# Kernel optimization log

Measured on AMD Instinct MI355X. Metric: run time of the kernel, lower is better.

Reference implementation:

```python
import jax, jax.numpy as jnp
import numpy as np

B, S, D, H, HD = 2, 2048, 1024, 16, 64


def setup_inputs() -> dict:
    key = jax.random.key(0)
    ks = jax.random.split(key, 11)
    scale_in = 1.0 / np.sqrt(D)
    return {
        "query": jax.random.normal(ks[0], (B, S, D), jnp.float32),
        "key": jax.random.normal(ks[1], (B, S, D), jnp.float32),
        "value": jax.random.normal(ks[2], (B, S, D), jnp.float32),
        "Wq": jax.random.normal(ks[3], (H, D, HD), jnp.float32) * scale_in,
        "bq": jax.random.normal(ks[4], (H, HD), jnp.float32) * 0.02,
        "Wk": jax.random.normal(ks[5], (H, D, HD), jnp.float32) * scale_in,
        "bk": jax.random.normal(ks[6], (H, HD), jnp.float32) * 0.02,
        "Wv": jax.random.normal(ks[7], (H, D, HD), jnp.float32) * scale_in,
        "bv": jax.random.normal(ks[8], (H, HD), jnp.float32) * 0.02,
        "Wo": jax.random.normal(ks[9], (D, D), jnp.float32) * scale_in,
        "bo": jax.random.normal(ks[10], (D,), jnp.float32) * 0.02,
    }


def reference(query, key, value, Wq, bq, Wk, bk, Wv, bv, Wo, bo):
    # Per-head projections, batched over heads (equivalent to the ModuleList loop).
    q = jnp.einsum('bsd,hdk->bhsk', query, Wq) + bq[None, :, None, :]   # [B,H,S,HD]
    k = jnp.einsum('bsd,hdk->bhsk', key, Wk) + bk[None, :, None, :]
    v = jnp.einsum('bsd,hdk->bhsk', value, Wv) + bv[None, :, None, :]
    scale = 1.0 / jnp.sqrt(jnp.asarray(q.shape[-1], q.dtype))
    scores = jnp.einsum('bhsk,bhtk->bhst', q, k) * scale                # [B,H,S,S]
    attn = jax.nn.softmax(scores, axis=-1)
    ctx = jnp.einsum('bhst,bhtk->bhsk', attn, v)                        # [B,H,S,HD]
    # Concat heads along last dim: [B,S,H*HD] == [B,S,D]
    x = jnp.transpose(ctx, (0, 2, 1, 3)).reshape(ctx.shape[0], ctx.shape[2], -1)
    return x @ Wo + bo
```

## Files before the change

### kernel.cpp

```cpp
#include <hip/hip_runtime.h>
#include <hip/hip_bf16.h>

typedef __bf16 bf16;
typedef __bf16 bf16x8 __attribute__((ext_vector_type(8)));
typedef __bf16 bf16x4 __attribute__((ext_vector_type(4)));
typedef __bf16 bf16x2 __attribute__((ext_vector_type(2)));
typedef float floatx4 __attribute__((ext_vector_type(4)));
typedef float floatx16 __attribute__((ext_vector_type(16)));

#define B_SZ 2
#define S_LEN 2048
#define D_DIM 1024
#define H_CNT 16
#define HD_DIM 64
#define M_ROWS 4096
#define QSCALE 0.18033688011112042f

__device__ __forceinline__ void async_ld16(const bf16* g, bf16* s) {
    __builtin_amdgcn_global_load_lds((const __attribute__((address_space(1))) void*)g,
                                     (__attribute__((address_space(3))) void*)s, 16, 0, 0);
}

__device__ __forceinline__ floatx4 mfma16(bf16x8 a, bf16x8 b, floatx4 c) {
    return __builtin_amdgcn_mfma_f32_16x16x32_bf16(a, b, c, 0, 0, 0);
}
__device__ __forceinline__ floatx16 mfma32(bf16x8 a, bf16x8 b, floatx16 c) {
    return __builtin_amdgcn_mfma_f32_32x32x16_bf16(a, b, c, 0, 0, 0);
}

struct PrepArgs {
    const float* cast_src[3]; bf16* cast_dst[3];
    const float* w_src[3];    bf16* w_dst[3];
    const float* wo;          bf16* wo_t;
};
__global__ __launch_bounds__(256) void prep(PrepArgs a) {
    __shared__ bf16 tile[32][33];
    const int bx = blockIdx.x, tid = threadIdx.x;
    if (bx < 12288) {
        const int t = bx >> 12, blk = bx & 4095;
        const float* s = a.cast_src[t];
        bf16* d = a.cast_dst[t];
        size_t i = ((size_t)blk * 256 + tid) * 4;
        float4 v = *(const float4*)(s + i);
        bf16x4 o = { (bf16)v.x, (bf16)v.y, (bf16)v.z, (bf16)v.w };
        *(bf16x4*)(d + i) = o;
        return;
    }
    int tx = tid & 31, ty = tid >> 5;
    const float* src; bf16* dst; int r0, c0, C, R;
    if (bx < 15360) {
        int idx = bx - 12288;
        int z = idx >> 6, xy = idx & 63;
        int mat = z >> 4, head = z & 15;
        src = a.w_src[mat] + (size_t)head * D_DIM * HD_DIM;
        dst = a.w_dst[mat] + (size_t)head * D_DIM * HD_DIM;
        r0 = (xy & 31) * 32; c0 = (xy >> 5) * 32; C = HD_DIM; R = D_DIM;
    } else {
        int idx = bx - 15360;
        src = a.wo; dst = a.wo_t;
        r0 = (idx & 31) * 32; c0 = (idx >> 5) * 32; C = D_DIM; R = D_DIM;
    }
#pragma unroll
    for (int i = 0; i < 32; i += 8)
        tile[ty + i][tx] = (bf16)src[(size_t)(r0 + ty + i) * C + c0 + tx];
    __syncthreads();
#pragma unroll
    for (int i = 0; i < 32; i += 8)
        dst[(size_t)(c0 + ty + i) * R + r0 + tx] = tile[tx][ty + i];
}

struct GemmPtrs { const bf16* A; const bf16* BT; const float* bias; bf16* C; float* Cf;
                  float scale; int mode; };
struct GemmArgs { GemmPtrs p[3]; };

__global__ __launch_bounds__(256) void gemm_bt(GemmArgs args) {
    __shared__ __align__(16) bf16 As[128 * 32];
    __shared__ __align__(16) bf16 Bs[128 * 32];
    const GemmPtrs P = args.p[blockIdx.z];
    const int tid = threadIdx.x, wave = tid >> 6, lane = tid & 63;
    const int quad = lane >> 4, l15 = lane & 15;
    const int bm = blockIdx.x * 128, bn = blockIdx.y * 128;
    const int wm = (wave >> 1) * 64, wn = (wave & 1) * 64;

    floatx4 acc[4][4];
#pragma unroll
    for (int i = 0; i < 4; i++)
#pragma unroll
        for (int j = 0; j < 4; j++) acc[i][j] = (floatx4){0.f, 0.f, 0.f, 0.f};

    const int srow = (lane >> 2);
    const int scol = (((lane & 3) ^ ((srow >> 1) & 3)) << 3);
    const int ck = ((quad ^ ((l15 >> 1) & 3)) << 3);
    for (int k0 = 0; k0 < 1024; k0 += 32) {
#pragma unroll
        for (int it = 0; it < 2; ++it) {
            int issue = it * 4 + wave;
            int row = issue * 16 + srow;
            async_ld16(P.A + (size_t)(bm + row) * 1024 + k0 + scol, &As[issue * 512]);
            async_ld16(P.BT + (size_t)(bn + row) * 1024 + k0 + scol, &Bs[issue * 512]);
        }
        __syncthreads();
        bf16x8 af[4], bfr[4];
#pragma unroll
        for (int mi = 0; mi < 4; mi++)
            af[mi] = *(const bf16x8*)&As[(wm + mi * 16 + l15) * 32 + ck];
#pragma unroll
        for (int ni = 0; ni < 4; ni++)
            bfr[ni] = *(const bf16x8*)&Bs[(wn + ni * 16 + l15) * 32 + ck];
#pragma unroll
        for (int mi = 0; mi < 4; mi++)
#pragma unroll
            for (int ni = 0; ni < 4; ni++) acc[mi][ni] = mfma16(af[mi], bfr[ni], acc[mi][ni]);
        __syncthreads();
    }
#pragma unroll
    for (int ni = 0; ni < 4; ni++) {
        int col = bn + wn + ni * 16 + l15;
        float bb = P.bias[col];
#pragma unroll
        for (int mi = 0; mi < 4; mi++) {
#pragma unroll
            for (int r = 0; r < 4; r++) {
                int row = bm + wm + mi * 16 + quad * 4 + r;
                float v = (acc[mi][ni][r] + bb) * P.scale;
                if (P.mode == 0) {
                    P.Cf[(size_t)row * 1024 + col] = v;
                } else {
                    int b = row >> 11, s2 = row & 2047, h = col >> 6, hd = col & 63;
                    if (P.mode == 1)
                        P.C[(((size_t)(b * H_CNT + h)) * S_LEN + s2) * HD_DIM + hd] = (bf16)v;
                    else
                        P.C[(((size_t)(b * H_CNT + h)) * HD_DIM + hd) * S_LEN + s2] = (bf16)v;
                }
            }
        }
    }
}

__global__ __launch_bounds__(256) void attn(const bf16* __restrict__ Qg, const bf16* __restrict__ Kg,
                                            const bf16* __restrict__ Vtg, bf16* __restrict__ ctx) {
    __shared__ __align__(16) bf16 Ks[2][8192];
    __shared__ __align__(16) bf16 Vs[2][8192];
    __shared__ __align__(16) bf16 Ps[4][2048];
    const int tid = threadIdx.x, wave = tid >> 6, lane = tid & 63;
    const int l31 = lane & 31, half = lane >> 5;
    const int bid = blockIdx.x;
    const int bh = (bid >> 1) & 31;
    const int qb = ((bid >> 6) << 1) | (bid & 1);
    const int q0blk = qb * 128;
    const bf16* Kp = Kg + (size_t)bh * S_LEN * HD_DIM;
    const bf16* Vp = Vtg + (size_t)bh * HD_DIM * S_LEN;

#pragma unroll
    for (int it = 0; it < 4; ++it) {
        int i = it * 4 + wave;
        int f = i * 512 + lane * 8;
        int sub = f >> 12, rem = f & 4095;
        int c = rem >> 9, r = (rem >> 3) & 63;
        async_ld16(Kp + (size_t)(sub * 64 + r) * HD_DIM + c * 8, &Ks[0][i * 512]);
        async_ld16(Vp + (size_t)r * S_LEN + sub * 64 + c * 8, &Vs[0][i * 512]);
    }
    bf16x8 qf[4];
    {
        const bf16* qrow = Qg + ((size_t)bh * S_LEN + q0blk + wave * 32 + l31) * HD_DIM;
#pragma unroll
        for (int kb = 0; kb < 4; ++kb)
            qf[kb] = *(const bf16x8*)(qrow + (2 * kb + half) * 8);
    }
    __syncthreads();

    bf16* Pw = Ps[wave];
    float l_i = 0.f;
    floatx16 o0 = {0}, o1 = {0};

    for (int rd = 0; rd < 16; ++rd) {
        const int cur = rd & 1;
        if (rd < 15) {
            int t0n = (rd + 1) * 128;
#pragma unroll
            for (int it = 0; it < 4; ++it) {
                int i = it * 4 + wave;
                int f = i * 512 + lane * 8;
                int sub = f >> 12, rem = f & 4095;
                int c = rem >> 9, r = (rem >> 3) & 63;
                async_ld16(Kp + (size_t)(t0n + sub * 64 + r) * HD_DIM + c * 8, &Ks[cur ^ 1][i * 512]);
                async_ld16(Vp + (size_t)r * S_LEN + t0n + sub * 64 + c * 8, &Vs[cur ^ 1][i * 512]);
            }
        }
#pragma unroll
        for (int sub = 0; sub < 2; ++sub) {
            const bf16* Kt = &Ks[cur][sub * 4096];
            const bf16* Vt = &Vs[cur][sub * 4096];
            floatx16 sc0 = {0}, sc1 = {0};
#pragma unroll
            for (int kb = 0; kb < 4; ++kb) {
                bf16x8 k0 = *(const bf16x8*)&Kt[(2 * kb + half) * 512 + l31 * 8];
                bf16x8 k1 = *(const bf16x8*)&Kt[(2 * kb + half) * 512 + (32 + l31) * 8];
                sc0 = mfma32(k0, qf[kb], sc0);
                sc1 = mfma32(k1, qf[kb], sc1);
            }
            float rs = 0.f;
#pragma unroll
            for (int e = 0; e < 16; e += 2) {
                float p0 = __builtin_amdgcn_exp2f(sc0[e]);
                float p1 = __builtin_amdgcn_exp2f(sc0[e + 1]);
                rs += p0 + p1;
                *(bf16x2*)&Pw[(e >> 2) * 256 + l31 * 8 + (e & 3) + 4 * half] = (bf16x2){(bf16)p0, (bf16)p1};
            }
#pragma unroll
            for (int e = 0; e < 16; e += 2) {
                float p0 = __builtin_amdgcn_exp2f(sc1[e]);
                float p1 = __builtin_amdgcn_exp2f(sc1[e + 1]);
                rs += p0 + p1;
                *(bf16x2*)&Pw[(4 + (e >> 2)) * 256 + l31 * 8 + (e & 3) + 4 * half] = (bf16x2){(bf16)p0, (bf16)p1};
            }
            l_i += rs;
#pragma unroll
            for (int kb = 0; kb < 4; ++kb) {
                bf16x8 pf = *(const bf16x8*)&Pw[(2 * kb + half) * 256 + l31 * 8];
                bf16x8 v0 = *(const bf16x8*)&Vt[(2 * kb + half) * 512 + l31 * 8];
                bf16x8 v1 = *(const bf16x8*)&Vt[(2 * kb + half) * 512 + (32 + l31) * 8];
                o0 = mfma32(v0, pf, o0);
                o1 = mfma32(v1, pf, o1);
            }
        }
        __syncthreads();
    }
    l_i += __shfl_xor(l_i, 32);
    int b = bh >> 4, hh = bh & 15;
    float inv = 1.f / l_i;
#pragma unroll
    for (int s2 = 0; s2 < 2; ++s2) {
        const floatx16 oo = s2 ? o1 : o0;
#pragma unroll
        for (int e = 0; e < 16; ++e) {
            int hd = (e & 3) + 8 * (e >> 2) + 4 * half;
            Pw[l31 * 40 + hd] = (bf16)(oo[e] * inv);
        }
#pragma unroll
        for (int p = 0; p < 2; ++p) {
            int q = p * 16 + (lane >> 2), part = lane & 3;
            bf16x8 v = *(const bf16x8*)&Pw[q * 40 + part * 8];
            int s = q0blk + wave * 32 + q;
            *(bf16x8*)&ctx[((size_t)(b * S_LEN + s)) * D_DIM + hh * 64 + s2 * 32 + part * 8] = v;
        }
    }
}

extern "C" void kernel_launch(void* const* d_in, const int* in_sizes, int n_in,
                              void* d_out, int out_size, void* d_ws, size_t ws_size,
                              hipStream_t stream) {
    const float* query = (const float*)d_in[0];
    const float* key   = (const float*)d_in[1];
    const float* value = (const float*)d_in[2];
    const float* Wq = (const float*)d_in[3];
    const float* bq = (const float*)d_in[4];
    const float* Wk = (const float*)d_in[5];
    const float* bk = (const float*)d_in[6];
    const float* Wv = (const float*)d_in[7];
    const float* bv = (const float*)d_in[8];
    const float* Wo = (const float*)d_in[9];
    const float* bo = (const float*)d_in[10];
    float* out = (float*)d_out;

    bf16* ws = (bf16*)d_ws;
    const size_t ASZ = (size_t)M_ROWS * D_DIM;
    const size_t WSZ = (size_t)H_CNT * D_DIM * HD_DIM;
    const size_t TSZ = (size_t)B_SZ * H_CNT * S_LEN * HD_DIM;
    bf16* Qc  = ws;
    bf16* Kc  = Qc + ASZ;
    bf16* Vc  = Kc + ASZ;
    bf16* WqT = Vc + ASZ;
    bf16* WkT = WqT + WSZ;
    bf16* WvT = WkT + WSZ;
    bf16* WoT = WvT + WSZ;
    bf16* Qb  = WoT + (size_t)D_DIM * D_DIM;
    bf16* Kb  = Qb + TSZ;
    bf16* Vtb = Kb + TSZ;
    bf16* ctx = Vtb + TSZ;

    dim3 blk(256);

    PrepArgs pa;
    pa.cast_src[0] = query; pa.cast_src[1] = key; pa.cast_src[2] = value;
    pa.cast_dst[0] = Qc;    pa.cast_dst[1] = Kc;  pa.cast_dst[2] = Vc;
    pa.w_src[0] = Wq; pa.w_src[1] = Wk; pa.w_src[2] = Wv;
    pa.w_dst[0] = WqT; pa.w_dst[1] = WkT; pa.w_dst[2] = WvT;
    pa.wo = Wo; pa.wo_t = WoT;
    prep<<<dim3(16384), blk, 0, stream>>>(pa);

    GemmArgs qkv;
    qkv.p[0] = {Qc, WqT, bq, Qb, nullptr, QSCALE, 1};
    qkv.p[1] = {Kc, WkT, bk, Kb, nullptr, 1.0f, 1};
    qkv.p[2] = {Vc, WvT, bv, Vtb, nullptr, 1.0f, 2};
    gemm_bt<<<dim3(32, 8, 3), blk, 0, stream>>>(qkv);

    attn<<<dim3(512), blk, 0, stream>>>(Qb, Kb, Vtb, ctx);

    GemmArgs og;
    og.p[0] = {ctx, WoT, bo, nullptr, out, 1.0f, 0};
    og.p[1] = og.p[0]; og.p[2] = og.p[0];
    gemm_bt<<<dim3(32, 8, 1), blk, 0, stream>>>(og);
}
```

Measured before the change: 236.5 us.

## Split attention KV range across two wave groups and keep P in registers

The attention kernel now runs 512 threads per block, and two groups of four waves each process half of the key/value sequence for the same 128 queries, 64 keys per round. Partial outputs and row sums are merged through shared memory at the end. The P matrix is no longer round-tripped through LDS; it is reshaped into MFMA operand layout in registers with v_permlane32_swap. s_setprio hints wrap the MFMA sections. These aim to cut LDS traffic and raise wave-level parallelism, at the cost of a shared-memory reduction epilogue and a sync every smaller step.

```diff
diff --git a/kernel.cpp b/kernel.cpp
--- a/kernel.cpp
+++ b/kernel.cpp
@@ -7,6 +7,7 @@
 typedef __bf16 bf16x2 __attribute__((ext_vector_type(2)));
 typedef float floatx4 __attribute__((ext_vector_type(4)));
 typedef float floatx16 __attribute__((ext_vector_type(16)));
+typedef int intx4 __attribute__((ext_vector_type(4)));
 
 #define B_SZ 2
 #define S_LEN 2048
@@ -26,6 +27,13 @@
 }
 __device__ __forceinline__ floatx16 mfma32(bf16x8 a, bf16x8 b, floatx16 c) {
     return __builtin_amdgcn_mfma_f32_32x32x16_bf16(a, b, c, 0, 0, 0);
+}
+
+__device__ __forceinline__ bf16x8 mkfrag(int a0, int a1, int b0, int b1) {
+    asm("v_permlane32_swap_b32 %0, %1" : "+v"(a0), "+v"(b0));
+    asm("v_permlane32_swap_b32 %0, %1" : "+v"(a1), "+v"(b1));
+    intx4 q = {a0, a1, b0, b1};
+    return __builtin_bit_cast(bf16x8, q);
 }
 
 struct PrepArgs {
@@ -137,112 +145,140 @@
     }
 }
 
-__global__ __launch_bounds__(256) void attn(const bf16* __restrict__ Qg, const bf16* __restrict__ Kg,
-                                            const bf16* __restrict__ Vtg, bf16* __restrict__ ctx) {
-    __shared__ __align__(16) bf16 Ks[2][8192];
-    __shared__ __align__(16) bf16 Vs[2][8192];
-    __shared__ __align__(16) bf16 Ps[4][2048];
+__global__ __launch_bounds__(512, 4) void attn(const bf16* __restrict__ Qg, const bf16* __restrict__ Kg,
+                                               const bf16* __restrict__ Vtg, bf16* __restrict__ ctx) {
+    __shared__ __align__(16) bf16 smem[32768];
     const int tid = threadIdx.x, wave = tid >> 6, lane = tid & 63;
     const int l31 = lane & 31, half = lane >> 5;
+    const int grp = wave >> 2, wg = wave & 3;
     const int bid = blockIdx.x;
     const int bh = (bid >> 1) & 31;
     const int qb = ((bid >> 6) << 1) | (bid & 1);
     const int q0blk = qb * 128;
     const bf16* Kp = Kg + (size_t)bh * S_LEN * HD_DIM;
     const bf16* Vp = Vtg + (size_t)bh * HD_DIM * S_LEN;
-
-#pragma unroll
-    for (int it = 0; it < 4; ++it) {
-        int i = it * 4 + wave;
-        int f = i * 512 + lane * 8;
-        int sub = f >> 12, rem = f & 4095;
-        int c = rem >> 9, r = (rem >> 3) & 63;
-        async_ld16(Kp + (size_t)(sub * 64 + r) * HD_DIM + c * 8, &Ks[0][i * 512]);
-        async_ld16(Vp + (size_t)r * S_LEN + sub * 64 + c * 8, &Vs[0][i * 512]);
-    }
+    const int tbase = grp * 1024;
+
+    const int f0 = wg * 512 + lane * 8, f1 = (wg + 4) * 512 + lane * 8;
+    const int kc0 = f0 >> 9, kt0 = (f0 >> 3) & 63;
+    const int kc1 = f1 >> 9, kt1 = (f1 >> 3) & 63;
+    bf16* const Kbase = smem + grp * 8192;
+    bf16* const Vbase = smem + 16384 + grp * 8192;
+
+#define STAGE(BUF, T0) do { \
+        bf16* Kd = Kbase + (BUF) * 4096; \
+        bf16* Vd = Vbase + (BUF) * 4096; \
+        async_ld16(Kp + (size_t)((T0) + kt0) * HD_DIM + kc0 * 8, Kd + wg * 512); \
+        async_ld16(Kp + (size_t)((T0) + kt1) * HD_DIM + kc1 * 8, Kd + (wg + 4) * 512); \
+        async_ld16(Vp + (size_t)kt0 * S_LEN + (T0) + kc0 * 8, Vd + wg * 512); \
+        async_ld16(Vp + (size_t)kt1 * S_LEN + (T0) + kc1 * 8, Vd + (wg + 4) * 512); \
+    } while (0)
+
+    STAGE(0, tbase);
     bf16x8 qf[4];
     {
-        const bf16* qrow = Qg + ((size_t)bh * S_LEN + q0blk + wave * 32 + l31) * HD_DIM;
+        const bf16* qrow = Qg + ((size_t)bh * S_LEN + q0blk + wg * 32 + l31) * HD_DIM;
 #pragma unroll
         for (int kb = 0; kb < 4; ++kb)
             qf[kb] = *(const bf16x8*)(qrow + (2 * kb + half) * 8);
     }
     __syncthreads();
 
-    bf16* Pw = Ps[wave];
     float l_i = 0.f;
     floatx16 o0 = {0}, o1 = {0};
 
     for (int rd = 0; rd < 16; ++rd) {
         const int cur = rd & 1;
-        if (rd < 15) {
-            int t0n = (rd + 1) * 128;
-#pragma unroll
-            for (int it = 0; it < 4; ++it) {
-                int i = it * 4 + wave;
-                int f = i * 512 + lane * 8;
-                int sub = f >> 12, rem = f & 4095;
-                int c = rem >> 9, r = (rem >> 3) & 63;
-                async_ld16(Kp + (size_t)(t0n + sub * 64 + r) * HD_DIM + c * 8, &Ks[cur ^ 1][i * 512]);
-                async_ld16(Vp + (size_t)r * S_LEN + t0n + sub * 64 + c * 8, &Vs[cur ^ 1][i * 512]);
+        if (rd < 15) STAGE(cur ^ 1, tbase + (rd + 1) * 64);
+        const bf16* Kt = Kbase + cur * 4096;
+        const bf16* Vt = Vbase + cur * 4096;
+        floatx16 sc0 = {0}, sc1 = {0};
+        __builtin_amdgcn_s_setprio(1);
+#pragma unroll
+        for (int kb = 0; kb < 4; ++kb) {
+            bf16x8 k0 = *(const bf16x8*)&Kt[(2 * kb + half) * 512 + l31 * 8];
+            bf16x8 k1 = *(const bf16x8*)&Kt[(2 * kb + half) * 512 + (32 + l31) * 8];
+            sc0 = mfma32(k0, qf[kb], sc0);
+            sc1 = mfma32(k1, qf[kb], sc1);
+        }
+        __builtin_amdgcn_s_setprio(0);
+        float rs = 0.f;
+        int w0[8], w1[8];
+#pragma unroll
+        for (int e = 0; e < 16; e += 2) {
+            float p0 = __builtin_amdgcn_exp2f(sc0[e]);
+            float p1 = __builtin_amdgcn_exp2f(sc0[e + 1]);
+            rs += p0 + p1;
+            bf16x2 t2 = {(bf16)p0, (bf16)p1};
+            w0[e >> 1] = __builtin_bit_cast(int, t2);
+        }
+#pragma unroll
+        for (int e = 0; e < 16; e += 2) {
+            float p0 = __builtin_amdgcn_exp2f(sc1[e]);
+            float p1 = __builtin_amdgcn_exp2f(sc1[e + 1]);
+            rs += p0 + p1;
+            bf16x2 t2 = {(bf16)p0, (bf16)p1};
+            w1[e >> 1] = __builtin_bit_cast(int, t2);
+        }
+        l_i += rs;
+        bf16x8 pfr[4];
+        pfr[0] = mkfrag(w0[0], w0[1], w0[2], w0[3]);
+        pfr[1] = mkfrag(w0[4], w0[5], w0[6], w0[7]);
+        pfr[2] = mkfrag(w1[0], w1[1], w1[2], w1[3]);
+        pfr[3] = mkfrag(w1[4], w1[5], w1[6], w1[7]);
+        __builtin_amdgcn_s_setprio(1);
+#pragma unroll
+        for (int kb = 0; kb < 4; ++kb) {
+            bf16x8 v0 = *(const bf16x8*)&Vt[(2 * kb + half) * 512 + l31 * 8];
+            bf16x8 v1 = *(const bf16x8*)&Vt[(2 * kb + half) * 512 + (32 + l31) * 8];
+            o0 = mfma32(v0, pfr[kb], o0);
+            o1 = mfma32(v1, pfr[kb], o1);
+        }
+        __builtin_amdgcn_s_setprio(0);
+        __syncthreads();
+    }
+#undef STAGE
+
+    l_i += __shfl_xor(l_i, 32);
+
+    float* slabF = (float*)smem;
+    float* lA = slabF + 4 * 2112;
+    if (grp == 0) {
+        float* S0 = slabF + wg * 2112;
+#pragma unroll
+        for (int s2 = 0; s2 < 2; ++s2) {
+            const floatx16 oo = s2 ? o1 : o0;
+#pragma unroll
+            for (int e = 0; e < 16; ++e) {
+                int hd = s2 * 32 + (e & 3) + 8 * (e >> 2) + 4 * half;
+                S0[l31 * 66 + hd] = oo[e];
             }
         }
-#pragma unroll
-        for (int sub = 0; sub < 2; ++sub) {
-            const bf16* Kt = &Ks[cur][sub * 4096];
-            const bf16* Vt = &Vs[cur][sub * 4096];
-            floatx16 sc0 = {0}, sc1 = {0};
-#pragma unroll
-            for (int kb = 0; kb < 4; ++kb) {
-                bf16x8 k0 = *(const bf16x8*)&Kt[(2 * kb + half) * 512 + l31 * 8];
-                bf16x8 k1 = *(const bf16x8*)&Kt[(2 * kb + half) * 512 + (32 + l31) * 8];
-                sc0 = mfma32(k0, qf[kb], sc0);
-                sc1 = mfma32(k1, qf[kb], sc1);
+        if (lane < 32) lA[wg * 32 + l31] = l_i;
+    }
+    __syncthreads();
+    if (grp == 1) {
+        float* S0 = slabF + wg * 2112;
+        float lt = l_i + lA[wg * 32 + l31];
+        float inv = 1.f / lt;
+        int b = bh >> 4, hh = bh & 15;
+        bf16* Sw = smem + 17408 + wg * 1280;
+#pragma unroll
+        for (int s2 = 0; s2 < 2; ++s2) {
+            const floatx16 oo = s2 ? o1 : o0;
+#pragma unroll
+            for (int e = 0; e < 16; ++e) {
+                int hd = (e & 3) + 8 * (e >> 2) + 4 * half;
+                float v = (oo[e] + S0[l31 * 66 + s2 * 32 + hd]) * inv;
+                Sw[l31 * 40 + hd] = (bf16)v;
             }
-            float rs = 0.f;
-#pragma unroll
-            for (int e = 0; e < 16; e += 2) {
-                float p0 = __builtin_amdgcn_exp2f(sc0[e]);
-                float p1 = __builtin_amdgcn_exp2f(sc0[e + 1]);
-                rs += p0 + p1;
-                *(bf16x2*)&Pw[(e >> 2) * 256 + l31 * 8 + (e & 3) + 4 * half] = (bf16x2){(bf16)p0, (bf16)p1};
+#pragma unroll
+            for (int p = 0; p < 2; ++p) {
+                int q = p * 16 + (lane >> 2), part = lane & 3;
+                bf16x8 v = *(const bf16x8*)&Sw[q * 40 + part * 8];
+                int s = q0blk + wg * 32 + q;
+                *(bf16x8*)&ctx[((size_t)(b * S_LEN + s)) * D_DIM + hh * 64 + s2 * 32 + part * 8] = v;
             }
-#pragma unroll
-            for (int e = 0; e < 16; e += 2) {
-                float p0 = __builtin_amdgcn_exp2f(sc1[e]);
-                float p1 = __builtin_amdgcn_exp2f(sc1[e + 1]);
-                rs += p0 + p1;
-                *(bf16x2*)&Pw[(4 + (e >> 2)) * 256 + l31 * 8 + (e & 3) + 4 * half] = (bf16x2){(bf16)p0, (bf16)p1};
-            }
-            l_i += rs;
-#pragma unroll
-            for (int kb = 0; kb < 4; ++kb) {
-                bf16x8 pf = *(const bf16x8*)&Pw[(2 * kb + half) * 256 + l31 * 8];
-                bf16x8 v0 = *(const bf16x8*)&Vt[(2 * kb + half) * 512 + l31 * 8];
-                bf16x8 v1 = *(const bf16x8*)&Vt[(2 * kb + half) * 512 + (32 + l31) * 8];
-                o0 = mfma32(v0, pf, o0);
-                o1 = mfma32(v1, pf, o1);
-            }
-        }
-        __syncthreads();
-    }
-    l_i += __shfl_xor(l_i, 32);
-    int b = bh >> 4, hh = bh & 15;
-    float inv = 1.f / l_i;
-#pragma unroll
-    for (int s2 = 0; s2 < 2; ++s2) {
-        const floatx16 oo = s2 ? o1 : o0;
-#pragma unroll
-        for (int e = 0; e < 16; ++e) {
-            int hd = (e & 3) + 8 * (e >> 2) + 4 * half;
-            Pw[l31 * 40 + hd] = (bf16)(oo[e] * inv);
-        }
-#pragma unroll
-        for (int p = 0; p < 2; ++p) {
-            int q = p * 16 + (lane >> 2), part = lane & 3;
-            bf16x8 v = *(const bf16x8*)&Pw[q * 40 + part * 8];
-            int s = q0blk + wave * 32 + q;
-            *(bf16x8*)&ctx[((size_t)(b * S_LEN + s)) * D_DIM + hh * 64 + s2 * 32 + part * 8] = v;
         }
     }
 }
@@ -295,7 +331,7 @@
     qkv.p[2] = {Vc, WvT, bv, Vtb, nullptr, 1.0f, 2};
     gemm_bt<<<dim3(32, 8, 3), blk, 0, stream>>>(qkv);
 
-    attn<<<dim3(512), blk, 0, stream>>>(Qb, Kb, Vtb, ctx);
+    attn<<<dim3(512), dim3(512), 0, stream>>>(Qb, Kb, Vtb, ctx);
 
     GemmArgs og;
     og.p[0] = {ctx, WoT, bo, nullptr, out, 1.0f, 0};
```

Measured after the change: 221.9 us. 6.2% less time.
